# Performance work log

Measured on AMD Instinct MI355X. Metric: run time of the kernel, lower is better.

The kernel has to match this reference:

```python
import jax, jax.numpy as jnp
import numpy as np

LN_EPS = 1e-5
NEG_SLOPE = 0.01  # torch LeakyReLU default


def layernorm(x, w, b):
    m = jnp.mean(x, axis=-1, keepdims=True)
    v = jnp.mean((x - m) ** 2, axis=-1, keepdims=True)
    return (x - m) * jax.lax.rsqrt(v + LN_EPS) * w + b


def setup_inputs() -> dict:
    key = jax.random.key(0)
    ks = jax.random.split(key, 12)
    B, T, C, E = 16, 1024, 768, 2
    d = C
    s = 0.02
    inp = {
        "x": jax.random.normal(ks[0], (B, T, C), jnp.float32),
        "ln1_w": jnp.ones((C,), jnp.float32),
        "ln1_b": jnp.zeros((C,), jnp.float32),
        "wqkv": jax.random.normal(ks[1], (C, 3 * C), jnp.float32) * s,
        "bqkv": jnp.zeros((3 * C,), jnp.float32),
        "wproj": jax.random.normal(ks[2], (C, C), jnp.float32) * s,
        "bproj": jnp.zeros((C,), jnp.float32),
        "ln2_w": jnp.ones((C,), jnp.float32),
        "ln2_b": jnp.zeros((C,), jnp.float32),
        "wg": jax.random.normal(ks[3], (C, E), jnp.float32) * s,
        # Experts module uses torch.randn (std 1); we scale down for numerics
        "w1": jax.random.normal(ks[4], (E, d, 4 * d), jnp.float32) * s,
        "w2": jax.random.normal(ks[5], (E, 4 * d, 4 * d), jnp.float32) * s,
        "w3": jax.random.normal(ks[6], (E, 4 * d, d), jnp.float32) * s,
        "n_head": 12,
    }
    return inp


def block_forward(x, ln1_w, ln1_b, wqkv, bqkv, wproj, bproj,
                  ln2_w, ln2_b, wg, w1, w2, w3, n_head):
    B, T, C = x.shape
    H = n_head
    hd = C // H
    E = wg.shape[-1]

    # ---- causal self-attention + residual ----
    h = layernorm(x, ln1_w, ln1_b)
    qkv = h @ wqkv + bqkv                      # [B,T,3C]
    q, k, v = jnp.split(qkv, 3, axis=-1)
    q = q.reshape(B, T, H, hd).transpose(0, 2, 1, 3)  # bhtd
    k = k.reshape(B, T, H, hd).transpose(0, 2, 1, 3)
    v = v.reshape(B, T, H, hd).transpose(0, 2, 1, 3)
    scores = jnp.einsum('bhqd,bhkd->bhqk', q, k) / jnp.sqrt(jnp.float32(hd))
    causal = jnp.tril(jnp.ones((T, T), bool))
    scores = jnp.where(causal, scores, jnp.finfo(scores.dtype).min)
    attn = jax.nn.softmax(scores, axis=-1)
    y = jnp.einsum('bhqk,bhkd->bhqd', attn, v)
    y = y.transpose(0, 2, 1, 3).reshape(B, T, C)
    x = x + (y @ wproj + bproj)

    # ---- MoE (top-2 gating, capacity dispatch) + residual ----
    h2 = layernorm(x, ln2_w, ln2_b)
    capacity = (T * 2) // E                    # capacity_factor = 1.0, top-2
    raw_gates = jax.nn.softmax(h2 @ wg, axis=-1)   # [B,T,E]

    idx1 = jnp.argmax(raw_gates, axis=-1)
    mask1 = jax.nn.one_hot(idx1, E, dtype=raw_gates.dtype)
    gate1 = jnp.sum(raw_gates * mask1, axis=-1)    # [B,T]
    gates2 = raw_gates * (1.0 - mask1)
    idx2 = jnp.argmax(gates2, axis=-1)
    mask2 = jax.nn.one_hot(idx2, E, dtype=raw_gates.dtype)
    gate2 = jnp.sum(raw_gates * mask2, axis=-1)
    denom = gate1 + gate2 + 1e-9
    gate1, gate2 = gate1 / denom, gate2 / denom

    # aux load-balancing loss (before capacity truncation)
    density = jnp.mean(mask1, axis=1)              # [B,E]
    density_proxy = jnp.mean(raw_gates, axis=1)    # [B,E]
    aux_loss = jnp.mean(density * density_proxy) * (E * E)

    # positions within each expert buffer (exclusive cumsum over tokens)
    pos1 = jnp.cumsum(mask1, axis=1) - mask1       # [B,T,E]
    mask1 = mask1 * (pos1 < capacity)
    mask1_count = jnp.sum(mask1, axis=1, keepdims=True)
    pos2 = (jnp.cumsum(mask2, axis=1) - mask2) + mask1_count
    mask2 = mask2 * (pos2 < capacity)

    oh1 = jax.nn.one_hot(pos1.astype(jnp.int32), capacity, dtype=raw_gates.dtype)
    oh2 = jax.nn.one_hot(pos2.astype(jnp.int32), capacity, dtype=raw_gates.dtype)
    combine = (gate1[..., None] * mask1)[..., None] * oh1 \
            + (gate2[..., None] * mask2)[..., None] * oh2   # [B,T,E,C]
    dispatch = (combine > 0).astype(h2.dtype)

    # dispatch -> per-expert batches
    expert_in = jnp.einsum('bnd,bnec->ebcd', h2, dispatch)   # [E,B,Cap,d]
    Bc = B * capacity
    ei = expert_in.reshape(E, Bc, C)
    lrelu = lambda z: jnp.where(z >= 0, z, NEG_SLOPE * z)
    hh = lrelu(jnp.einsum('end,edh->enh', ei, w1))
    hh = lrelu(jnp.einsum('end,edh->enh', hh, w2))
    eo = jnp.einsum('end,edh->enh', hh, w3).reshape(E, B, capacity, C)
    moe_out = jnp.einsum('ebcd,bnec->bnd', eo, combine)

    x = x + moe_out
    return x, aux_loss


def reference(x, ln1_w, ln1_b, wqkv, bqkv, wproj, bproj,
              ln2_w, ln2_b, wg, w1, w2, w3, n_head):
    return block_forward(x, ln1_w, ln1_b, wqkv, bqkv, wproj, bproj,
                         ln2_w, ln2_b, wg, w1, w2, w3, n_head)
```

## Files before the change

kernel.cpp:

```cpp
#include <hip/hip_runtime.h>
#include <cstdint>
#include <cstddef>

constexpr int B_  = 16;
constexpr int T_  = 1024;
constexpr int C_  = 768;
constexpr int H_  = 12;
constexpr int HD_ = 64;
constexpr int BT_ = B_ * T_;
constexpr int C3_ = 3 * C_;
constexpr int FF_ = 4 * C_;
constexpr int MCH_ = 8192;

typedef __bf16 bf16x8 __attribute__((ext_vector_type(8)));
typedef float  floatx4 __attribute__((ext_vector_type(4)));
typedef unsigned short u16x8 __attribute__((ext_vector_type(8)));

__device__ inline float bf2f(unsigned short u) {
  union { unsigned int i; float f; } x; x.i = ((unsigned int)u) << 16; return x.f;
}
__device__ inline unsigned short f2bf(float f) {
  union { float f; unsigned int i; } x; x.f = f;
  unsigned int u = x.i;
  u += 0x7fffu + ((u >> 16) & 1u);
  return (unsigned short)(u >> 16);
}

#define GLOAD_LDS16(gp, lp)                                              \
  __builtin_amdgcn_global_load_lds(                                      \
      (__attribute__((address_space(1))) void*)(gp),                     \
      (__attribute__((address_space(3))) void*)(lp), 16, 0, 0)

__launch_bounds__(256)
__global__ void ln_kernel(const float* __restrict__ x, const float* __restrict__ w,
                          const float* __restrict__ b, unsigned short* __restrict__ out) {
  int row = blockIdx.x;
  int tid = threadIdx.x;
  const float* xr = x + (size_t)row * C_;
  float v0 = xr[tid], v1 = xr[tid + 256], v2 = xr[tid + 512];
  float s  = v0 + v1 + v2;
  float ss = v0 * v0 + v1 * v1 + v2 * v2;
#pragma unroll
  for (int off = 32; off > 0; off >>= 1) {
    s  += __shfl_down(s, off, 64);
    ss += __shfl_down(ss, off, 64);
  }
  __shared__ float red[8];
  int wid = tid >> 6;
  if ((tid & 63) == 0) { red[wid] = s; red[4 + wid] = ss; }
  __syncthreads();
  float st  = red[0] + red[1] + red[2] + red[3];
  float sst = red[4] + red[5] + red[6] + red[7];
  float mean = st * (1.0f / C_);
  float var  = sst * (1.0f / C_) - mean * mean;
  float rstd = rsqrtf(var + 1e-5f);
  unsigned short* orow = out + (size_t)row * C_;
  orow[tid]       = f2bf((v0 - mean) * rstd * w[tid]       + b[tid]);
  orow[tid + 256] = f2bf((v1 - mean) * rstd * w[tid + 256] + b[tid + 256]);
  orow[tid + 512] = f2bf((v2 - mean) * rstd * w[tid + 512] + b[tid + 512]);
}

__launch_bounds__(256)
__global__ void convT(const float* __restrict__ in, unsigned short* __restrict__ out,
                      int K, int N) {
  __shared__ float t[32][33];
  int n0 = blockIdx.x * 32, k0 = blockIdx.y * 32;
  int tx = threadIdx.x & 31, ty = threadIdx.x >> 5;
#pragma unroll
  for (int r = 0; r < 32; r += 8)
    t[r + ty][tx] = in[(size_t)(k0 + r + ty) * N + n0 + tx];
  __syncthreads();
#pragma unroll
  for (int r = 0; r < 32; r += 8)
    out[(size_t)(n0 + r + ty) * K + k0 + tx] = f2bf(t[tx][r + ty]);
}

template <int ACT, bool BIAS, bool RES, bool COMBINE, bool OUTBF16>
__launch_bounds__(256)
__global__ void gemm_bf16(const unsigned short* __restrict__ A,
                          const unsigned short* __restrict__ Bt,
                          const float* __restrict__ bias,
                          const float* __restrict__ Rres,
                          const float* __restrict__ gates2, int eidx,
                          void* __restrict__ Cout,
                          int M, int N, int K) {
  __shared__ __attribute__((aligned(16))) unsigned short Als[8192];
  __shared__ __attribute__((aligned(16))) unsigned short Bls[8192];
  const int tid  = threadIdx.x;
  const int wave = tid >> 6, lane = tid & 63;
  const int wr = wave >> 1, wc = wave & 1;
  const int m0 = blockIdx.y * 128, n0 = blockIdx.x * 128;

  const int srow = wave * 32 + (lane >> 3);
  const int skg  = (lane & 7) ^ ((lane >> 3) & 7);
  const unsigned short* Ap = A  + (size_t)(m0 + srow) * K + skg * 8;
  const unsigned short* Bp = Bt + (size_t)(n0 + srow) * K + skg * 8;
  unsigned short* AlsW = Als + wave * 2048;
  unsigned short* BlsW = Bls + wave * 2048;

  floatx4 acc[4][4];
#pragma unroll
  for (int i = 0; i < 4; ++i)
#pragma unroll
    for (int j = 0; j < 4; ++j) acc[i][j] = floatx4{0.f, 0.f, 0.f, 0.f};

  const int q  = lane >> 4;
  const int ml = lane & 15;
  const int rsw = ml & 7;

  for (int k0 = 0; k0 < K; k0 += 64) {
    __syncthreads();
#pragma unroll
    for (int i = 0; i < 4; ++i) {
      GLOAD_LDS16(Ap + (size_t)(i * 8) * K + k0, AlsW + i * 512);
      GLOAD_LDS16(Bp + (size_t)(i * 8) * K + k0, BlsW + i * 512);
    }
    __syncthreads();
#pragma unroll
    for (int ks = 0; ks < 2; ++ks) {
      const int p = (ks * 4 + q) ^ rsw;
      bf16x8 af[4], bfg[4];
#pragma unroll
      for (int i = 0; i < 4; ++i) {
        int ar = wr * 64 + i * 16 + ml;
        af[i]  = *(const bf16x8*)&Als[(ar * 8 + p) * 8];
        int br = wc * 64 + i * 16 + ml;
        bfg[i] = *(const bf16x8*)&Bls[(br * 8 + p) * 8];
      }
#pragma unroll
      for (int i = 0; i < 4; ++i)
#pragma unroll
        for (int j = 0; j < 4; ++j)
          acc[i][j] = __builtin_amdgcn_mfma_f32_16x16x32_bf16(af[i], bfg[j], acc[i][j], 0, 0, 0);
    }
  }

  const int rbase = q * 4;
#pragma unroll
  for (int i = 0; i < 4; ++i) {
    int row = m0 + wr * 64 + i * 16 + rbase;
#pragma unroll
    for (int j = 0; j < 4; ++j) {
      int col = n0 + wc * 64 + j * 16 + ml;
      float bcol = BIAS ? bias[col] : 0.f;
#pragma unroll
      for (int r = 0; r < 4; ++r) {
        float v = acc[i][j][r];
        if (BIAS) v += bcol;
        if (ACT == 1) v = (v >= 0.f) ? v : 0.01f * v;
        if (RES) v += Rres[(size_t)(row + r) * N + col];
        if (COMBINE) {
          float g = gates2[2 * (row + r) + eidx];
          float* op = (float*)Cout + (size_t)(row + r) * N + col;
          *op += g * v;
        } else if (OUTBF16) {
          ((unsigned short*)Cout)[(size_t)(row + r) * N + col] = f2bf(v);
        } else {
          ((float*)Cout)[(size_t)(row + r) * N + col] = v;
        }
      }
    }
  }
}

__launch_bounds__(256)
__global__ void attn_kernel(const unsigned short* __restrict__ qkv,
                            unsigned short* __restrict__ y) {
  __shared__ __attribute__((aligned(16))) unsigned short Qls[64 * 64];
  __shared__ __attribute__((aligned(16))) unsigned short Kls[64 * 64];
  __shared__ __attribute__((aligned(16))) unsigned short Vt[64 * 72];
  __shared__ __attribute__((aligned(16))) unsigned short Pls[4 * 16 * 72];

  const int tid  = threadIdx.x;
  const int wave = tid >> 6, lane = tid & 63;
  const int quad = lane >> 4, n = lane & 15;
  const int q0 = blockIdx.x * 64;
  const int bh = blockIdx.y;
  const int b = bh / H_, h = bh % H_;
  const size_t base = (size_t)b * T_ * C3_ + (size_t)h * HD_;

  {
    const int r8 = lane >> 3;
    const int g  = (lane & 7) ^ r8;
#pragma unroll
    for (int i = 0; i < 2; ++i) {
      int row = wave * 16 + i * 8 + r8;
      GLOAD_LDS16(qkv + base + (size_t)(q0 + row) * C3_ + g * 8,
                  Qls + wave * 1024 + i * 512);
    }
  }

  floatx4 O[4];
#pragma unroll
  for (int ct = 0; ct < 4; ++ct) O[ct] = floatx4{0.f, 0.f, 0.f, 0.f};
  float mrow[4] = {-1e30f, -1e30f, -1e30f, -1e30f};
  float lrow[4] = {0.f, 0.f, 0.f, 0.f};

  const int nkt = blockIdx.x + 1;
  unsigned short* Pw = Pls + wave * (16 * 72);

  for (int kt = 0; kt < nkt; ++kt) {
    const int k0 = kt << 6;
    __syncthreads();
    {
      const int r8 = lane >> 3;
      const int g  = (lane & 7) ^ r8;
#pragma unroll
      for (int i = 0; i < 2; ++i) {
        int key = wave * 16 + i * 8 + r8;
        GLOAD_LDS16(qkv + base + (size_t)(k0 + key) * C3_ + C_ + g * 8,
                    Kls + wave * 1024 + i * 512);
      }
    }
    {
      int key = tid & 63;
      int dbase = (tid >> 6) * 8;
#pragma unroll
      for (int it = 0; it < 2; ++it) {
        int d0 = dbase + it * 32;
        u16x8 vv = *(const u16x8*)(qkv + base + (size_t)(k0 + key) * C3_ + 2 * C_ + d0);
#pragma unroll
        for (int j = 0; j < 8; ++j) Vt[(d0 + j) * 72 + key] = vv[j];
      }
    }
    __syncthreads();

    floatx4 sacc[4];
#pragma unroll
    for (int ct = 0; ct < 4; ++ct) sacc[ct] = floatx4{0.f, 0.f, 0.f, 0.f};
#pragma unroll
    for (int ks = 0; ks < 2; ++ks) {
      const int ga = (ks * 4 + quad) ^ (n & 7);
      bf16x8 aq = *(const bf16x8*)&Qls[((wave * 16 + n) * 8 + ga) * 8];
#pragma unroll
      for (int ct = 0; ct < 4; ++ct) {
        bf16x8 kb = *(const bf16x8*)&Kls[((ct * 16 + n) * 8 + ga) * 8];
        sacc[ct] = __builtin_amdgcn_mfma_f32_16x16x32_bf16(aq, kb, sacc[ct], 0, 0, 0);
      }
    }

    float p[4][4];
#pragma unroll
    for (int ct = 0; ct < 4; ++ct)
#pragma unroll
      for (int r = 0; r < 4; ++r) p[ct][r] = sacc[ct][r] * 0.125f;
    if (kt == nkt - 1) {
      const int kgb = k0 + n, qgb = q0 + wave * 16 + quad * 4;
#pragma unroll
      for (int ct = 0; ct < 4; ++ct)
#pragma unroll
        for (int r = 0; r < 4; ++r)
          if (kgb + ct * 16 > qgb + r) p[ct][r] = -1e30f;
    }
#pragma unroll
    for (int r = 0; r < 4; ++r) {
      float tm = fmaxf(fmaxf(p[0][r], p[1][r]), fmaxf(p[2][r], p[3][r]));
      tm = fmaxf(tm, __shfl_xor(tm, 1, 64));
      tm = fmaxf(tm, __shfl_xor(tm, 2, 64));
      tm = fmaxf(tm, __shfl_xor(tm, 4, 64));
      tm = fmaxf(tm, __shfl_xor(tm, 8, 64));
      float mn = fmaxf(mrow[r], tm);
      float alpha = __expf(mrow[r] - mn);
      mrow[r] = mn;
      float ps = 0.f;
#pragma unroll
      for (int ct = 0; ct < 4; ++ct) {
        float pe = __expf(p[ct][r] - mn);
        p[ct][r] = pe;
        ps += pe;
      }
      ps += __shfl_xor(ps, 1, 64);
      ps += __shfl_xor(ps, 2, 64);
      ps += __shfl_xor(ps, 4, 64);
      ps += __shfl_xor(ps, 8, 64);
      lrow[r] = lrow[r] * alpha + ps;
      O[0][r] *= alpha; O[1][r] *= alpha; O[2][r] *= alpha; O[3][r] *= alpha;
    }

#pragma unroll
    for (int ct = 0; ct < 4; ++ct)
#pragma unroll
      for (int r = 0; r < 4; ++r)
        Pw[(quad * 4 + r) * 72 + ct * 16 + n] = f2bf(p[ct][r]);

#pragma unroll
    for (int ks = 0; ks < 2; ++ks) {
      bf16x8 pa = *(const bf16x8*)&Pw[n * 72 + (ks * 4 + quad) * 8];
#pragma unroll
      for (int ct = 0; ct < 4; ++ct) {
        bf16x8 vb = *(const bf16x8*)&Vt[(ct * 16 + n) * 72 + (ks * 4 + quad) * 8];
        O[ct] = __builtin_amdgcn_mfma_f32_16x16x32_bf16(pa, vb, O[ct], 0, 0, 0);
      }
    }
  }

#pragma unroll
  for (int r = 0; r < 4; ++r) {
    float inv = 1.0f / lrow[r];
    int row = q0 + wave * 16 + quad * 4 + r;
    unsigned short* dst = y + ((size_t)b * T_ + row) * C_ + h * HD_;
#pragma unroll
    for (int ct = 0; ct < 4; ++ct)
      dst[ct * 16 + n] = f2bf(O[ct][r] * inv);
  }
}

__launch_bounds__(256)
__global__ void gate_kernel(const unsigned short* __restrict__ h2,
                            const float* __restrict__ wg,
                            float* __restrict__ gates) {
  int wave = threadIdx.x >> 6, lane = threadIdx.x & 63;
  int t = blockIdx.x * 4 + wave;
  const unsigned short* hr = h2 + (size_t)t * C_;
  float a0 = 0.0f, a1 = 0.0f;
#pragma unroll
  for (int i = 0; i < 12; ++i) {
    int d = lane + 64 * i;
    float hv = bf2f(hr[d]);
    a0 += hv * wg[2 * d];
    a1 += hv * wg[2 * d + 1];
  }
#pragma unroll
  for (int off = 32; off > 0; off >>= 1) {
    a0 += __shfl_down(a0, off, 64);
    a1 += __shfl_down(a1, off, 64);
  }
  if (lane == 0) {
    float m  = fmaxf(a0, a1);
    float e0 = __expf(a0 - m), e1 = __expf(a1 - m);
    float invs = 1.0f / (e0 + e1);
    float p0 = e0 * invs, p1 = e1 * invs;
    const float gnorm = 1.0f / (1.0f + 1e-9f);
    gates[2 * t]     = p0 * gnorm;
    gates[2 * t + 1] = p1 * gnorm;
  }
}

__launch_bounds__(1024)
__global__ void moe_stats_kernel(const float* __restrict__ gates,
                                 float* __restrict__ out_aux) {
  int wave = threadIdx.x >> 6, lane = threadIdx.x & 63;
  float c0 = 0.f, sp0 = 0.f, sp1 = 0.f;
#pragma unroll
  for (int j = 0; j < 16; ++j) {
    int t = wave * T_ + lane + 64 * j;
    float p0 = gates[2 * t], p1 = gates[2 * t + 1];
    c0  += (p1 > p0) ? 0.f : 1.f;
    sp0 += p0;
    sp1 += p1;
  }
#pragma unroll
  for (int off = 32; off > 0; off >>= 1) {
    c0  += __shfl_down(c0, off, 64);
    sp0 += __shfl_down(sp0, off, 64);
    sp1 += __shfl_down(sp1, off, 64);
  }
  __shared__ float red[16][3];
  if (lane == 0) { red[wave][0] = c0; red[wave][1] = sp0; red[wave][2] = sp1; }
  __syncthreads();
  if (threadIdx.x == 0) {
    float s = 0.f;
    for (int b = 0; b < B_; ++b) {
      float cc0 = red[b][0];
      float d0 = cc0 * (1.f / T_), d1 = (T_ - cc0) * (1.f / T_);
      float px0 = red[b][1] * (1.f / T_), px1 = red[b][2] * (1.f / T_);
      s += d0 * px0 + d1 * px1;
    }
    out_aux[0] = s * (4.f / 32.f);
  }
}

extern "C" void kernel_launch(void* const* d_in, const int* in_sizes, int n_in,
                              void* d_out, int out_size, void* d_ws, size_t ws_size,
                              hipStream_t stream) {
  const float* x     = (const float*)d_in[0];
  const float* ln1_w = (const float*)d_in[1];
  const float* ln1_b = (const float*)d_in[2];
  const float* wqkv  = (const float*)d_in[3];
  const float* bqkv  = (const float*)d_in[4];
  const float* wproj = (const float*)d_in[5];
  const float* bproj = (const float*)d_in[6];
  const float* ln2_w = (const float*)d_in[7];
  const float* ln2_b = (const float*)d_in[8];
  const float* wg    = (const float*)d_in[9];
  const float* w1    = (const float*)d_in[10];
  const float* w2    = (const float*)d_in[11];
  const float* w3    = (const float*)d_in[12];
  float* out = (float*)d_out;

  unsigned short* wsu   = (unsigned short*)d_ws;
  unsigned short* wqkvT = wsu;
  unsigned short* wprojT= wqkvT + (size_t)C3_ * C_;
  unsigned short* w1T   = wprojT + (size_t)C_ * C_;
  unsigned short* w2T   = w1T + (size_t)2 * FF_ * C_;
  unsigned short* w3T   = w2T + (size_t)2 * FF_ * FF_;
  unsigned short* hb    = w3T + (size_t)2 * C_ * FF_;
  unsigned short* region= hb + (size_t)BT_ * C_;
  unsigned short* qkvb  = region;
  unsigned short* yb    = region + (size_t)BT_ * C3_;
  unsigned short* hh1   = region;
  unsigned short* hh2   = region + (size_t)MCH_ * FF_;
  float* gates = (float*)(region + (size_t)BT_ * 4 * C_);

  convT<<<dim3(C3_ / 32, C_ / 32), 256, 0, stream>>>(wqkv, wqkvT, C_, C3_);
  convT<<<dim3(C_ / 32, C_ / 32), 256, 0, stream>>>(wproj, wprojT, C_, C_);
  for (int e = 0; e < 2; ++e) {
    convT<<<dim3(FF_ / 32, C_ / 32), 256, 0, stream>>>(
        w1 + (size_t)e * C_ * FF_, w1T + (size_t)e * FF_ * C_, C_, FF_);
    convT<<<dim3(FF_ / 32, FF_ / 32), 256, 0, stream>>>(
        w2 + (size_t)e * FF_ * FF_, w2T + (size_t)e * FF_ * FF_, FF_, FF_);
    convT<<<dim3(C_ / 32, FF_ / 32), 256, 0, stream>>>(
        w3 + (size_t)e * FF_ * C_, w3T + (size_t)e * C_ * FF_, FF_, C_);
  }

  ln_kernel<<<BT_, 256, 0, stream>>>(x, ln1_w, ln1_b, hb);
  gemm_bf16<0, true, false, false, true><<<dim3(C3_ / 128, BT_ / 128), 256, 0, stream>>>(
      hb, wqkvT, bqkv, nullptr, nullptr, 0, qkvb, BT_, C3_, C_);
  attn_kernel<<<dim3(T_ / 64, B_ * H_), 256, 0, stream>>>(qkvb, yb);
  gemm_bf16<0, true, true, false, false><<<dim3(C_ / 128, BT_ / 128), 256, 0, stream>>>(
      yb, wprojT, bproj, x, nullptr, 0, out, BT_, C_, C_);

  ln_kernel<<<BT_, 256, 0, stream>>>(out, ln2_w, ln2_b, hb);
  gate_kernel<<<BT_ / 4, 256, 0, stream>>>(hb, wg, gates);
  moe_stats_kernel<<<1, 1024, 0, stream>>>(gates, out + (size_t)BT_ * C_);

  for (int e = 0; e < 2; ++e) {
    for (int c = 0; c < BT_ / MCH_; ++c) {
      const unsigned short* a = hb + (size_t)c * MCH_ * C_;
      gemm_bf16<1, false, false, false, true><<<dim3(FF_ / 128, MCH_ / 128), 256, 0, stream>>>(
          a, w1T + (size_t)e * FF_ * C_, nullptr, nullptr, nullptr, 0, hh1, MCH_, FF_, C_);
      gemm_bf16<1, false, false, false, true><<<dim3(FF_ / 128, MCH_ / 128), 256, 0, stream>>>(
          hh1, w2T + (size_t)e * FF_ * FF_, nullptr, nullptr, nullptr, 0, hh2, MCH_, FF_, FF_);
      gemm_bf16<0, false, false, true, false><<<dim3(C_ / 128, MCH_ / 128), 256, 0, stream>>>(
          hh2, w3T + (size_t)e * C_ * FF_, nullptr, nullptr,
          gates + (size_t)2 * c * MCH_, e, out + (size_t)c * MCH_ * C_, MCH_, C_, FF_);
    }
  }
}
```

Measured before the change: 1.781 ms.

## Add 256x256-tile 512-thread GEMM with direct-to-LDS pipelining for QKV and MoE FFN

```diff
diff --git a/kernel.cpp b/kernel.cpp
--- a/kernel.cpp
+++ b/kernel.cpp
@@ -161,6 +161,128 @@
       }
     }
   }
+}
+
+#define GB256_BAR()   asm volatile("s_barrier" ::: "memory")
+#define GB256_LGKM0() asm volatile("s_waitcnt lgkmcnt(0)" ::: "memory")
+
+template <int ACT, bool BIAS>
+__launch_bounds__(512, 2)
+__global__ void gemm256(const unsigned short* __restrict__ A,
+                        const unsigned short* __restrict__ Bt,
+                        const float* __restrict__ bias,
+                        unsigned short* __restrict__ Cout,
+                        int M, int N, int K) {
+  __shared__ __attribute__((aligned(16))) unsigned short L[65536];
+  const int tid = threadIdx.x;
+  const int w = tid >> 6, l = tid & 63;
+  const int wr = w >> 2, wc = w & 3;
+  const int ml = l & 15, q = l >> 4;
+  const int m0 = blockIdx.y * 256, n0 = blockIdx.x * 256;
+
+  const int srow = l >> 2;
+  const int sg   = ((l & 3) ^ ((l >> 3) & 3)) * 8;
+  const unsigned short* Ast = A  + (size_t)(m0 + srow) * K + sg;
+  const unsigned short* Bst = Bt + (size_t)(n0 + srow) * K + sg;
+  const int ldsw = w * 1024;
+
+#define STG(cb, mat, ks, srcp, kk)                                           \
+  do {                                                                       \
+    const unsigned short* _s = (srcp) + (size_t)(w * 32) * K + (kk) + (ks) * 32; \
+    unsigned short* _d = L + (cb) * 32768 + (mat) * 16384 + (ks) * 8192 + ldsw;  \
+    GLOAD_LDS16(_s, _d);                                                     \
+    GLOAD_LDS16(_s + (size_t)16 * K, _d + 512);                              \
+  } while (0)
+
+  const int dphys = (q ^ ((ml >> 1) & 3)) * 8;
+  const int aoff = (wr * 128 + ml) * 32 + dphys;
+  const int boff = (wc * 64 + ml) * 32 + dphys;
+
+  floatx4 acc[8][4];
+#pragma unroll
+  for (int m = 0; m < 8; ++m)
+#pragma unroll
+    for (int n = 0; n < 4; ++n) acc[m][n] = floatx4{0.f, 0.f, 0.f, 0.f};
+
+  const int NT = K >> 6;
+
+  STG(0, 0, 0, Ast, 0);  STG(0, 1, 0, Bst, 0);
+  STG(0, 0, 1, Ast, 0);  STG(0, 1, 1, Bst, 0);
+  STG(1, 0, 0, Ast, 64); STG(1, 1, 0, Bst, 64);
+  asm volatile("s_waitcnt vmcnt(0)" ::: "memory");
+  GB256_BAR();
+
+  for (int j = 0; j < NT; ++j) {
+    const int c = j & 1, nx = c ^ 1;
+    const int kk1 = (j + 1) << 6, kk2 = (j + 2) << 6;
+    const bool st1 = (j + 1 < NT), st2 = (j + 2 < NT);
+    bf16x8 bA[4], bB[4];
+
+#define LOAD_A(KS, MH)                                                       \
+  _Pragma("unroll")                                                          \
+  for (int mq = 0; mq < 4; ++mq)                                             \
+    bA[mq] = *(const bf16x8*)&L[c * 32768 + (KS) * 8192 + aoff + ((MH) * 4 + mq) * 512];
+#define LOAD_B(KS)                                                           \
+  _Pragma("unroll")                                                          \
+  for (int n = 0; n < 4; ++n)                                                \
+    bB[n] = *(const bf16x8*)&L[c * 32768 + 16384 + (KS) * 8192 + boff + n * 512];
+#define MFMA16(MH)                                                           \
+  __builtin_amdgcn_s_setprio(1);                                             \
+  _Pragma("unroll")                                                          \
+  for (int mq = 0; mq < 4; ++mq)                                             \
+    _Pragma("unroll")                                                        \
+    for (int n = 0; n < 4; ++n)                                              \
+      acc[(MH) * 4 + mq][n] = __builtin_amdgcn_mfma_f32_16x16x32_bf16(       \
+          bA[mq], bB[n], acc[(MH) * 4 + mq][n], 0, 0, 0);                    \
+  __builtin_amdgcn_s_setprio(0);
+
+    LOAD_B(0); LOAD_A(0, 0);
+    if (st1) STG(nx, 0, 1, Ast, kk1);
+    GB256_BAR(); GB256_LGKM0();
+    MFMA16(0);
+    GB256_BAR();
+
+    LOAD_A(0, 1);
+    if (st1) STG(nx, 1, 1, Bst, kk1);
+    GB256_BAR(); GB256_LGKM0();
+    MFMA16(1);
+    GB256_BAR();
+
+    LOAD_B(1); LOAD_A(1, 0);
+    if (st2) STG(c, 0, 0, Ast, kk2);
+    GB256_BAR(); GB256_LGKM0();
+    MFMA16(0);
+    GB256_BAR();
+
+    LOAD_A(1, 1);
+    if (st2) STG(c, 1, 0, Bst, kk2);
+    GB256_BAR(); GB256_LGKM0();
+    MFMA16(1);
+    if (st2)      asm volatile("s_waitcnt vmcnt(4)" ::: "memory");
+    else if (st1) asm volatile("s_waitcnt vmcnt(0)" ::: "memory");
+    GB256_BAR();
+#undef LOAD_A
+#undef LOAD_B
+#undef MFMA16
+  }
+
+#pragma unroll
+  for (int m = 0; m < 8; ++m) {
+    const int row = m0 + wr * 128 + m * 16 + q * 4;
+#pragma unroll
+    for (int n = 0; n < 4; ++n) {
+      const int col = n0 + wc * 64 + n * 16 + ml;
+      const float bcol = BIAS ? bias[col] : 0.f;
+#pragma unroll
+      for (int r = 0; r < 4; ++r) {
+        float v = acc[m][n][r];
+        if (BIAS) v += bcol;
+        if (ACT == 1) v = (v >= 0.f) ? v : 0.01f * v;
+        Cout[(size_t)(row + r) * N + col] = f2bf(v);
+      }
+    }
+  }
+#undef STG
 }
 
 __launch_bounds__(256)
@@ -414,8 +536,8 @@
   }
 
   ln_kernel<<<BT_, 256, 0, stream>>>(x, ln1_w, ln1_b, hb);
-  gemm_bf16<0, true, false, false, true><<<dim3(C3_ / 128, BT_ / 128), 256, 0, stream>>>(
-      hb, wqkvT, bqkv, nullptr, nullptr, 0, qkvb, BT_, C3_, C_);
+  gemm256<0, true><<<dim3(C3_ / 256, BT_ / 256), 512, 0, stream>>>(
+      hb, wqkvT, bqkv, qkvb, BT_, C3_, C_);
   attn_kernel<<<dim3(T_ / 64, B_ * H_), 256, 0, stream>>>(qkvb, yb);
   gemm_bf16<0, true, true, false, false><<<dim3(C_ / 128, BT_ / 128), 256, 0, stream>>>(
       yb, wprojT, bproj, x, nullptr, 0, out, BT_, C_, C_);
@@ -427,10 +549,10 @@
   for (int e = 0; e < 2; ++e) {
     for (int c = 0; c < BT_ / MCH_; ++c) {
       const unsigned short* a = hb + (size_t)c * MCH_ * C_;
-      gemm_bf16<1, false, false, false, true><<<dim3(FF_ / 128, MCH_ / 128), 256, 0, stream>>>(
-          a, w1T + (size_t)e * FF_ * C_, nullptr, nullptr, nullptr, 0, hh1, MCH_, FF_, C_);
-      gemm_bf16<1, false, false, false, true><<<dim3(FF_ / 128, MCH_ / 128), 256, 0, stream>>>(
-          hh1, w2T + (size_t)e * FF_ * FF_, nullptr, nullptr, nullptr, 0, hh2, MCH_, FF_, FF_);
+      gemm256<1, false><<<dim3(FF_ / 256, MCH_ / 256), 512, 0, stream>>>(
+          a, w1T + (size_t)e * FF_ * C_, nullptr, hh1, MCH_, FF_, C_);
+      gemm256<1, false><<<dim3(FF_ / 256, MCH_ / 256), 512, 0, stream>>>(
+          hh1, w2T + (size_t)e * FF_ * FF_, nullptr, hh2, MCH_, FF_, FF_);
       gemm_bf16<0, false, false, true, false><<<dim3(C_ / 128, MCH_ / 128), 256, 0, stream>>>(
           hh2, w3T + (size_t)e * C_ * FF_, nullptr, nullptr,
           gates + (size_t)2 * c * MCH_, e, out + (size_t)c * MCH_ * C_, MCH_, C_, FF_);
```

Result: slower. 1.820 ms (+2.2%).
